# Kernel optimization log

Hardware: AMD Instinct MI355X
Metric: run time of the kernel (lower is better)

The kernel has to match this reference:

```python
import jax, jax.numpy as jnp
import numpy as np

B, NW, H, K = 64, 256, 768, 4
K1, Bp, AVDL = 0.1, 1.2, 50.0
ALPHA = 1.0 / H  # 1 / interaction_rep_size
BETA = 0.1


def setup_inputs() -> dict:
    key = jax.random.key(0)
    k1, k2, k3, k4, k5, k6 = jax.random.split(key, 6)
    return {
        "q_rep": jax.random.normal(k1, (B, NW, H), dtype=jnp.float32),
        "d_rep": jax.random.normal(k2, (B, NW, H), dtype=jnp.float32),
        "qtw": jax.random.uniform(k3, (B, NW), dtype=jnp.float32),
        "q_input_ids": jax.random.randint(k4, (B, NW, K), 0, 32, dtype=jnp.int32),
        "d_input_ids": jax.random.randint(k5, (B, NW, K), 0, 32, dtype=jnp.int32),
        "d_tfs": jax.random.randint(k6, (B, NW), 0, 10, dtype=jnp.int32),
    }


def _null_mask(input_ids):
    # [B, NW, 1] float mask: 0 where the whole window is zero ids
    all_zero = jnp.all(input_ids == 0, axis=2)
    return (~all_zero).astype(jnp.float32)[:, :, None]


def reference(q_rep, d_rep, qtw, q_input_ids, d_input_ids, d_tfs):
    q = q_rep * _null_mask(q_input_ids)
    d = d_rep * _null_mask(d_input_ids)

    # term-overlap scores: [B, NW, NW]
    d_expanded_tf = jnp.einsum("bqh,bdh->bqd", q, d)

    # exact match between q windows and d windows: [B, NW, NW]
    em_f = jnp.all(q_input_ids[:, :, None, :] == d_input_ids[:, None, :, :],
                   axis=3).astype(jnp.float32)

    # blended expanded term frequency, weighted by doc term frequencies
    d_tf = d_expanded_tf * (ALPHA * BETA) + em_f * (1.0 - BETA)
    tf_mult = d_tfs.astype(jnp.float32)[:, None, :]          # [B, 1, NW]
    expanded_term_df = jnp.sum(d_tf * tf_mult, axis=2)       # [B, NW]

    # BM25-like scoring
    dl = jnp.sum(d_tfs.astype(jnp.float32), axis=1, keepdims=True)  # [B, 1]
    denom = expanded_term_df * (1.0 + K1)
    nom = expanded_term_df + K1 * (1.0 - Bp + Bp * dl / AVDL)
    dtw = denom / (nom + 1e-8)
    s = jnp.sum(qtw * dtw, axis=1)                           # [B]
    return s, d_expanded_tf
```

## Files before the change

### kernel.cpp

```cpp
#include <hip/hip_runtime.h>
#include <hip/hip_bf16.h>

#define B_   64
#define NW_  256
#define H_   768

#define AB_    (0.1f / 768.0f)
#define OMB_   0.9f
#define K1_    0.1f
#define BP_    1.2f
#define AVDL_  50.0f

typedef __bf16 bf16x4 __attribute__((ext_vector_type(4)));
typedef __bf16 bf16x8 __attribute__((ext_vector_type(8)));
typedef float  f32x4  __attribute__((ext_vector_type(4)));

__global__ __launch_bounds__(256, 1) void gemm_fused(
    const float* __restrict__ q_rep, const float* __restrict__ d_rep,
    const int* __restrict__ q_ids, const int* __restrict__ d_ids,
    const int* __restrict__ d_tfs,
    float* __restrict__ S, float* __restrict__ ws_dot)
{
    __shared__ __align__(16) __bf16 As[2][128][40];
    __shared__ __align__(16) __bf16 Bs[2][128][40];
    __shared__ float mq_s[128];
    __shared__ float md_s[128];
    __shared__ float mdtf_s[128];

    const int tid  = threadIdx.x;
    const int wave = tid >> 6;
    const int lane = tid & 63;
    const int bid  = blockIdx.x;
    const int b    = bid & 63;
    const int t    = bid >> 6;
    const int m0   = (t & 1) * 128;
    const int n0   = (t >> 1) * 128;

    if (tid < 128) {
        int4 qa = *(const int4*)(q_ids + ((size_t)b * NW_ + m0 + tid) * 4);
        mq_s[tid] = (qa.x == 0 && qa.y == 0 && qa.z == 0 && qa.w == 0) ? 0.f : 1.f;
    } else {
        const int r = tid - 128;
        int4 da = *(const int4*)(d_ids + ((size_t)b * NW_ + n0 + r) * 4);
        float md = (da.x == 0 && da.y == 0 && da.z == 0 && da.w == 0) ? 0.f : 1.f;
        md_s[r]   = md;
        mdtf_s[r] = md * (float)d_tfs[(size_t)b * NW_ + n0 + r];
    }

    const int srow = tid >> 3;
    const int sseg = tid & 7;
    const float* Abase = q_rep + ((size_t)b * NW_ + m0) * H_;
    const float* Bbase = d_rep + ((size_t)b * NW_ + n0) * H_;

    float4 ra[4], rb[4];
    auto loadg = [&](int kc) {
#pragma unroll
        for (int i = 0; i < 4; ++i) {
            const int row = i * 32 + srow;
            ra[i] = *(const float4*)(Abase + (size_t)row * H_ + kc * 32 + sseg * 4);
            rb[i] = *(const float4*)(Bbase + (size_t)row * H_ + kc * 32 + sseg * 4);
        }
    };
    auto stage = [&](int buf) {
#pragma unroll
        for (int i = 0; i < 4; ++i) {
            const int row = i * 32 + srow;
            bf16x4 va = { (__bf16)ra[i].x, (__bf16)ra[i].y,
                          (__bf16)ra[i].z, (__bf16)ra[i].w };
            *(bf16x4*)&As[buf][row][sseg * 4] = va;
            bf16x4 vb = { (__bf16)rb[i].x, (__bf16)rb[i].y,
                          (__bf16)rb[i].z, (__bf16)rb[i].w };
            *(bf16x4*)&Bs[buf][row][sseg * 4] = vb;
        }
    };

    f32x4 acc[4][4];
#pragma unroll
    for (int i = 0; i < 4; ++i)
#pragma unroll
        for (int j = 0; j < 4; ++j)
            acc[i][j] = (f32x4){0.f, 0.f, 0.f, 0.f};

    const int fr = lane & 15;
    const int fk = (lane >> 4) * 8;
    const int qm = wave >> 1;
    const int qn = wave & 1;

    loadg(0);
    stage(0);
    __syncthreads();

    for (int kc = 0; kc < 24; ++kc) {
        const int buf = kc & 1;
        if (kc < 23) loadg(kc + 1);
        bf16x8 af[4], bfr[4];
#pragma unroll
        for (int t4 = 0; t4 < 4; ++t4) {
            af[t4]  = *(bf16x8*)&As[buf][qm * 64 + t4 * 16 + fr][fk];
            bfr[t4] = *(bf16x8*)&Bs[buf][qn * 64 + t4 * 16 + fr][fk];
        }
#pragma unroll
        for (int i = 0; i < 4; ++i)
#pragma unroll
            for (int j = 0; j < 4; ++j)
                acc[i][j] = __builtin_amdgcn_mfma_f32_16x16x32_bf16(
                    af[i], bfr[j], acc[i][j], 0, 0, 0);
        if (kc < 23) stage(buf ^ 1);
        __syncthreads();
    }

    const int cn = lane & 15;
    const int qg = lane >> 4;
    float md_l[4], mdtf_l[4];
#pragma unroll
    for (int j = 0; j < 4; ++j) {
        const int c = qn * 64 + j * 16 + cn;
        md_l[j]   = md_s[c];
        mdtf_l[j] = mdtf_s[c];
    }
    float* Sbase = S + ((size_t)b * NW_ + m0 + qm * 64) * NW_ + n0 + qn * 64;

    float rs[16];
#pragma unroll
    for (int i = 0; i < 4; ++i)
#pragma unroll
        for (int r = 0; r < 4; ++r) {
            const int row = i * 16 + qg * 4 + r;
            const float mq = mq_s[qm * 64 + row];
            float s = 0.f;
#pragma unroll
            for (int j = 0; j < 4; ++j) {
                const float v = acc[i][j][r];
                Sbase[(size_t)row * NW_ + j * 16 + cn] = v * mq * md_l[j];
                s += v * mdtf_l[j];
            }
            rs[i * 4 + r] = s;
        }
#pragma unroll
    for (int off = 1; off <= 8; off <<= 1)
#pragma unroll
        for (int e = 0; e < 16; ++e)
            rs[e] += __shfl_xor(rs[e], off);
    if (cn == 0) {
#pragma unroll
        for (int i = 0; i < 4; ++i)
#pragma unroll
            for (int r = 0; r < 4; ++r)
                atomicAdd(&ws_dot[(size_t)b * NW_ + m0 + qm * 64 + i * 16 + qg * 4 + r],
                          rs[i * 4 + r]);
    }
}

__global__ __launch_bounds__(256) void final_kernel(
    const float* __restrict__ ws_dot, const int* __restrict__ q_ids,
    const int* __restrict__ d_ids, const int* __restrict__ d_tfs,
    const float* __restrict__ qtw, float* __restrict__ out)
{
    __shared__ int4  dk_s[256];
    __shared__ float tf_s[256];
    __shared__ float red[4];

    const int b = blockIdx.x;
    const int t = threadIdx.x;
    const int wave = t >> 6;
    const int lane = t & 63;

    dk_s[t] = *(const int4*)(d_ids + ((size_t)b * NW_ + t) * 4);
    tf_s[t] = (float)d_tfs[(size_t)b * NW_ + t];
    __syncthreads();

    const int4 qk = *(const int4*)(q_ids + ((size_t)b * NW_ + t) * 4);
    float em = 0.f, dl = 0.f;
    for (int d = 0; d < 256; ++d) {
        const int4 dk = dk_s[d];
        const float tf = tf_s[d];
        dl += tf;
        if (dk.x == qk.x && dk.y == qk.y && dk.z == qk.z && dk.w == qk.w)
            em += tf;
    }
    const float mq = (qk.x | qk.y | qk.z | qk.w) ? 1.f : 0.f;
    const float etdf = AB_ * mq * ws_dot[(size_t)b * NW_ + t] + OMB_ * em;
    const float c = K1_ * (1.f - BP_ + BP_ * dl / AVDL_);
    float val = qtw[(size_t)b * NW_ + t] * (etdf * (1.f + K1_)) / (etdf + c + 1e-8f);

#pragma unroll
    for (int off = 32; off; off >>= 1) val += __shfl_xor(val, off);
    if (lane == 0) red[wave] = val;
    __syncthreads();
    if (t == 0) out[b] = red[0] + red[1] + red[2] + red[3];
}

extern "C" void kernel_launch(void* const* d_in, const int* in_sizes, int n_in,
                              void* d_out, int out_size, void* d_ws, size_t ws_size,
                              hipStream_t stream)
{
    const float* q_rep = (const float*)d_in[0];
    const float* d_rep = (const float*)d_in[1];
    const float* qtw   = (const float*)d_in[2];
    const int*   q_ids = (const int*)d_in[3];
    const int*   d_ids = (const int*)d_in[4];
    const int*   d_tfs = (const int*)d_in[5];

    float* out = (float*)d_out;
    float* S   = out + B_;
    float* ws_dot = (float*)d_ws;

    hipMemsetAsync(ws_dot, 0, (size_t)B_ * NW_ * sizeof(float), stream);

    gemm_fused<<<256, 256, 0, stream>>>(q_rep, d_rep, q_ids, d_ids, d_tfs,
                                        S, ws_dot);
    final_kernel<<<B_, 256, 0, stream>>>(ws_dot, q_ids, d_ids, d_tfs, qtw, out);
}
```

Measured before the change: 176.4 us.

## Prefetch three k-chunks ahead and fuse exact-match scoring into GEMM epilogue

```diff
diff --git a/kernel.cpp b/kernel.cpp
--- a/kernel.cpp
+++ b/kernel.cpp
@@ -15,17 +15,22 @@
 typedef __bf16 bf16x8 __attribute__((ext_vector_type(8)));
 typedef float  f32x4  __attribute__((ext_vector_type(4)));
 
+#define BAR_LGKM() asm volatile("s_waitcnt lgkmcnt(0)\n\ts_barrier" ::: "memory")
+
 __global__ __launch_bounds__(256, 1) void gemm_fused(
     const float* __restrict__ q_rep, const float* __restrict__ d_rep,
     const int* __restrict__ q_ids, const int* __restrict__ d_ids,
     const int* __restrict__ d_tfs,
-    float* __restrict__ S, float* __restrict__ ws_dot)
+    float* __restrict__ S, float* __restrict__ ws_etdf)
 {
     __shared__ __align__(16) __bf16 As[2][128][40];
     __shared__ __align__(16) __bf16 Bs[2][128][40];
     __shared__ float mq_s[128];
     __shared__ float md_s[128];
     __shared__ float mdtf_s[128];
+    __shared__ float tf_s[128];
+    __shared__ int4  qk_s[128];
+    __shared__ int4  dk_s[128];
 
     const int tid  = threadIdx.x;
     const int wave = tid >> 6;
@@ -38,13 +43,17 @@
 
     if (tid < 128) {
         int4 qa = *(const int4*)(q_ids + ((size_t)b * NW_ + m0 + tid) * 4);
+        qk_s[tid] = qa;
         mq_s[tid] = (qa.x == 0 && qa.y == 0 && qa.z == 0 && qa.w == 0) ? 0.f : 1.f;
     } else {
         const int r = tid - 128;
         int4 da = *(const int4*)(d_ids + ((size_t)b * NW_ + n0 + r) * 4);
+        dk_s[r] = da;
         float md = (da.x == 0 && da.y == 0 && da.z == 0 && da.w == 0) ? 0.f : 1.f;
+        float tf = (float)d_tfs[(size_t)b * NW_ + n0 + r];
         md_s[r]   = md;
-        mdtf_s[r] = md * (float)d_tfs[(size_t)b * NW_ + n0 + r];
+        tf_s[r]   = tf;
+        mdtf_s[r] = md * tf;
     }
 
     const int srow = tid >> 3;
@@ -52,8 +61,9 @@
     const float* Abase = q_rep + ((size_t)b * NW_ + m0) * H_;
     const float* Bbase = d_rep + ((size_t)b * NW_ + n0) * H_;
 
-    float4 ra[4], rb[4];
-    auto loadg = [&](int kc) {
+    float4 ra0[4], rb0[4], ra1[4], rb1[4], ra2[4], rb2[4];
+
+    auto loadg = [&](float4 (&ra)[4], float4 (&rb)[4], int kc) {
 #pragma unroll
         for (int i = 0; i < 4; ++i) {
             const int row = i * 32 + srow;
@@ -61,7 +71,7 @@
             rb[i] = *(const float4*)(Bbase + (size_t)row * H_ + kc * 32 + sseg * 4);
         }
     };
-    auto stage = [&](int buf) {
+    auto stage = [&](float4 (&ra)[4], float4 (&rb)[4], int buf) {
 #pragma unroll
         for (int i = 0; i < 4; ++i) {
             const int row = i * 32 + srow;
@@ -86,13 +96,20 @@
     const int qm = wave >> 1;
     const int qn = wave & 1;
 
-    loadg(0);
-    stage(0);
-    __syncthreads();
-
+    loadg(ra0, rb0, 0);
+    loadg(ra1, rb1, 1);
+    loadg(ra2, rb2, 2);
+    stage(ra0, rb0, 0);
+    BAR_LGKM();
+
+#pragma unroll
     for (int kc = 0; kc < 24; ++kc) {
         const int buf = kc & 1;
-        if (kc < 23) loadg(kc + 1);
+        if (kc < 21) {
+            if (kc % 3 == 0)      loadg(ra0, rb0, kc + 3);
+            else if (kc % 3 == 1) loadg(ra1, rb1, kc + 3);
+            else                  loadg(ra2, rb2, kc + 3);
+        }
         bf16x8 af[4], bfr[4];
 #pragma unroll
         for (int t4 = 0; t4 < 4; ++t4) {
@@ -105,18 +122,26 @@
             for (int j = 0; j < 4; ++j)
                 acc[i][j] = __builtin_amdgcn_mfma_f32_16x16x32_bf16(
                     af[i], bfr[j], acc[i][j], 0, 0, 0);
-        if (kc < 23) stage(buf ^ 1);
-        __syncthreads();
+        if (kc < 23) {
+            const int nb = buf ^ 1;
+            if ((kc + 1) % 3 == 0)      stage(ra0, rb0, nb);
+            else if ((kc + 1) % 3 == 1) stage(ra1, rb1, nb);
+            else                        stage(ra2, rb2, nb);
+        }
+        BAR_LGKM();
     }
 
     const int cn = lane & 15;
     const int qg = lane >> 4;
-    float md_l[4], mdtf_l[4];
+    float md_l[4], mdtf_l[4], tf_l[4];
+    int4  dk_l[4];
 #pragma unroll
     for (int j = 0; j < 4; ++j) {
         const int c = qn * 64 + j * 16 + cn;
         md_l[j]   = md_s[c];
         mdtf_l[j] = mdtf_s[c];
+        tf_l[j]   = tf_s[c];
+        dk_l[j]   = dk_s[c];
     }
     float* Sbase = S + ((size_t)b * NW_ + m0 + qm * 64) * NW_ + n0 + qn * 64;
 
@@ -127,14 +152,18 @@
         for (int r = 0; r < 4; ++r) {
             const int row = i * 16 + qg * 4 + r;
             const float mq = mq_s[qm * 64 + row];
-            float s = 0.f;
+            const int4  qk = qk_s[qm * 64 + row];
+            float sdot = 0.f, sem = 0.f;
 #pragma unroll
             for (int j = 0; j < 4; ++j) {
                 const float v = acc[i][j][r];
                 Sbase[(size_t)row * NW_ + j * 16 + cn] = v * mq * md_l[j];
-                s += v * mdtf_l[j];
+                sdot += v * mdtf_l[j];
+                const int4 dk = dk_l[j];
+                if (dk.x == qk.x && dk.y == qk.y && dk.z == qk.z && dk.w == qk.w)
+                    sem += tf_l[j];
             }
-            rs[i * 4 + r] = s;
+            rs[i * 4 + r] = mq * AB_ * sdot + OMB_ * sem;
         }
 #pragma unroll
     for (int off = 1; off <= 8; off <<= 1)
@@ -146,48 +175,36 @@
         for (int i = 0; i < 4; ++i)
 #pragma unroll
             for (int r = 0; r < 4; ++r)
-                atomicAdd(&ws_dot[(size_t)b * NW_ + m0 + qm * 64 + i * 16 + qg * 4 + r],
+                atomicAdd(&ws_etdf[(size_t)b * NW_ + m0 + qm * 64 + i * 16 + qg * 4 + r],
                           rs[i * 4 + r]);
     }
 }
 
-__global__ __launch_bounds__(256) void final_kernel(
-    const float* __restrict__ ws_dot, const int* __restrict__ q_ids,
-    const int* __restrict__ d_ids, const int* __restrict__ d_tfs,
+__global__ __launch_bounds__(64) void final_kernel(
+    const float* __restrict__ ws_etdf, const int* __restrict__ d_tfs,
     const float* __restrict__ qtw, float* __restrict__ out)
 {
-    __shared__ int4  dk_s[256];
-    __shared__ float tf_s[256];
-    __shared__ float red[4];
-
     const int b = blockIdx.x;
-    const int t = threadIdx.x;
-    const int wave = t >> 6;
-    const int lane = t & 63;
-
-    dk_s[t] = *(const int4*)(d_ids + ((size_t)b * NW_ + t) * 4);
-    tf_s[t] = (float)d_tfs[(size_t)b * NW_ + t];
-    __syncthreads();
-
-    const int4 qk = *(const int4*)(q_ids + ((size_t)b * NW_ + t) * 4);
-    float em = 0.f, dl = 0.f;
-    for (int d = 0; d < 256; ++d) {
-        const int4 dk = dk_s[d];
-        const float tf = tf_s[d];
-        dl += tf;
-        if (dk.x == qk.x && dk.y == qk.y && dk.z == qk.z && dk.w == qk.w)
-            em += tf;
-    }
-    const float mq = (qk.x | qk.y | qk.z | qk.w) ? 1.f : 0.f;
-    const float etdf = AB_ * mq * ws_dot[(size_t)b * NW_ + t] + OMB_ * em;
+    const int lane = threadIdx.x;
+
+    float4 ev = *(const float4*)(ws_etdf + (size_t)b * NW_ + lane * 4);
+    int4  tf4 = *(const int4*)(d_tfs   + (size_t)b * NW_ + lane * 4);
+    float4 qv = *(const float4*)(qtw    + (size_t)b * NW_ + lane * 4);
+
+    float dl = (float)(tf4.x + tf4.y + tf4.z + tf4.w);
+#pragma unroll
+    for (int off = 32; off; off >>= 1) dl += __shfl_xor(dl, off);
+
     const float c = K1_ * (1.f - BP_ + BP_ * dl / AVDL_);
-    float val = qtw[(size_t)b * NW_ + t] * (etdf * (1.f + K1_)) / (etdf + c + 1e-8f);
-
-#pragma unroll
-    for (int off = 32; off; off >>= 1) val += __shfl_xor(val, off);
-    if (lane == 0) red[wave] = val;
-    __syncthreads();
-    if (t == 0) out[b] = red[0] + red[1] + red[2] + red[3];
+    float ew[4] = {ev.x, ev.y, ev.z, ev.w};
+    float qw[4] = {qv.x, qv.y, qv.z, qv.w};
+    float s = 0.f;
+#pragma unroll
+    for (int j = 0; j < 4; ++j)
+        s += qw[j] * (ew[j] * (1.f + K1_)) / (ew[j] + c + 1e-8f);
+#pragma unroll
+    for (int off = 32; off; off >>= 1) s += __shfl_xor(s, off);
+    if (lane == 0) out[b] = s;
 }
 
 extern "C" void kernel_launch(void* const* d_in, const int* in_sizes, int n_in,
@@ -203,11 +220,11 @@
 
     float* out = (float*)d_out;
     float* S   = out + B_;
-    float* ws_dot = (float*)d_ws;
-
-    hipMemsetAsync(ws_dot, 0, (size_t)B_ * NW_ * sizeof(float), stream);
+    float* ws_etdf = (float*)d_ws;
+
+    hipMemsetAsync(ws_etdf, 0, (size_t)B_ * NW_ * sizeof(float), stream);
 
     gemm_fused<<<256, 256, 0, stream>>>(q_rep, d_rep, q_ids, d_ids, d_tfs,
-                                        S, ws_dot);
-    final_kernel<<<B_, 256, 0, stream>>>(ws_dot, q_ids, d_ids, d_tfs, qtw, out);
+                                        S, ws_etdf);
+    final_kernel<<<B_, 64, 0, stream>>>(ws_etdf, d_tfs, qtw, out);
 }
```

After: 147.2 us. 16.6% less time.
